# Kernel tuning notes

Hardware: AMD Instinct MI355X
Metric: run time of the kernel (lower is better)

## Reference

```python
import jax, jax.numpy as jnp
import numpy as np

KS = 3      # kernel size
PAD = 1     # zero padding
STRIDE = 1
N = KS * KS # 9 sampling points per pixel


def _deform_conv(feature, offset, weight):
    """DeformConv2d: bilinear sample at learned offsets then 3x3 conv (no bias)."""
    b, c, h, w = feature.shape
    x = jnp.pad(feature, ((0, 0), (0, 0), (PAD, PAD), (PAD, PAD)))
    hp, wp = h + 2 * PAD, w + 2 * PAD
    dt = feature.dtype
    # p_n: kernel grid offsets, x(rows) first then y(cols) -> (2N,)
    rng = jnp.arange(-(KS - 1) // 2, (KS - 1) // 2 + 1, dtype=dt)
    pn_x, pn_y = jnp.meshgrid(rng, rng, indexing='ij')
    # p_0: base sampling grid starting at 1 (accounts for zero padding)
    p0_x, p0_y = jnp.meshgrid(jnp.arange(1, h + 1, dtype=dt),
                              jnp.arange(1, w + 1, dtype=dt), indexing='ij')
    # sampling locations p = p_0 + p_n + offset, split into x/y -> (b,h,w,N)
    off = jnp.transpose(offset, (0, 2, 3, 1))  # (b,h,w,2N)
    px = p0_x[None, :, :, None] + pn_x.reshape(-1)[None, None, None, :] + off[..., :N]
    py = p0_y[None, :, :, None] + pn_y.reshape(-1)[None, None, None, :] + off[..., N:]
    q_lt_x = jnp.clip(jnp.floor(px), 0, hp - 1)
    q_lt_y = jnp.clip(jnp.floor(py), 0, wp - 1)
    q_rb_x = jnp.clip(jnp.floor(px) + 1, 0, hp - 1)
    q_rb_y = jnp.clip(jnp.floor(py) + 1, 0, wp - 1)
    px = jnp.clip(px, 0, hp - 1)
    py = jnp.clip(py, 0, wp - 1)
    # bilinear weights for the 4 corners
    g_lt = (1 + (q_lt_x - px)) * (1 + (q_lt_y - py))
    g_rb = (1 - (q_rb_x - px)) * (1 - (q_rb_y - py))
    g_lb = (1 + (q_lt_x - px)) * (1 - (q_rb_y - py))
    g_rt = (1 - (q_rb_x - px)) * (1 + (q_lt_y - py))
    x_flat = x.reshape(b, c, hp * wp)

    def gather(qx, qy):
        idx = (qx * wp + qy).astype(jnp.int32).reshape(b, 1, -1)
        v = jnp.take_along_axis(x_flat, jnp.broadcast_to(idx, (b, c, h * w * N)), axis=2)
        return v.reshape(b, c, h, w, N)

    x_off = (g_lt[:, None] * gather(q_lt_x, q_lt_y)
             + g_rb[:, None] * gather(q_rb_x, q_rb_y)
             + g_lb[:, None] * gather(q_lt_x, q_rb_y)
             + g_rt[:, None] * gather(q_rb_x, q_lt_y))  # (b,c,h,w,N)
    # equivalent of _reshape_x_offset + conv(ks, stride=ks)
    x_off = x_off.reshape(b, c, h, w, KS, KS)
    return jnp.einsum('bchwij,ocij->bohw', x_off, weight)


def setup_inputs() -> dict:
    key = jax.random.key(0)
    k1, k2, k3 = jax.random.split(key, 3)
    B, C, H, W = 4, 256, 64, 64
    feature = jax.random.normal(k1, (B, C, H, W), dtype=jnp.float32)
    offset = jax.random.normal(k2, (B, 2 * N, H, W), dtype=jnp.float32)
    weight = jax.random.normal(k3, (C, C, KS, KS), dtype=jnp.float32) / np.sqrt(C * N)
    return {"feature": feature, "offset": offset, "weight": weight}


def reference(feature, offset, weight):
    f1 = jax.nn.relu(_deform_conv(feature, offset, weight))
    return jax.nn.relu(f1 + feature)
```

## Files before the change

### kernel.cpp

```cpp
#include <hip/hip_runtime.h>

#define HW    4096
#define J_TOT 16384
#define K_TOT 2304
#define C_CH  256

typedef unsigned short u16;
typedef unsigned int   u32;
typedef __attribute__((ext_vector_type(8))) short short8;
typedef __attribute__((ext_vector_type(4))) float f32x4;
typedef __attribute__((ext_vector_type(8))) unsigned short us8;

__device__ __forceinline__ float b2f(u16 u) { return __uint_as_float(((u32)u) << 16); }
__device__ __forceinline__ u16 f2b(float x) {
  u32 u = __float_as_uint(x);
  u += 0x7FFFu + ((u >> 16) & 1u);
  return (u16)(u >> 16);
}

__device__ __forceinline__ void gload_lds16(const u16* g, u16* l) {
  __builtin_amdgcn_global_load_lds(
      (__attribute__((address_space(1))) void*)(void*)g,
      (__attribute__((address_space(3))) void*)(void*)l, 16, 0, 0);
}

__global__ void k_detect(const u16* __restrict__ f, int* __restrict__ flag) {
  __shared__ int sh[256];
  int t = threadIdx.x;
  int hits = 0;
  for (int i = t; i < 2048; i += 256) {
    u16 u = f[2 * i];
    int e = (u >> 7) & 0xFF;
    hits += (e >= 100 && e <= 141) ? 1 : 0;
  }
  sh[t] = hits;
  __syncthreads();
  if (t == 0) {
    int s = 0;
    for (int i = 0; i < 256; i++) s += sh[i];
    flag[0] = (s > 1024) ? 1 : 0;
  }
}

__global__ void k_transpose(const void* __restrict__ featv, u16* __restrict__ ftr,
                            const int* __restrict__ flag) {
  __shared__ u16 tile[32][33];
  int isbf = *flag;
  int b = blockIdx.z;
  int hw0 = blockIdx.x << 5;
  int c0 = blockIdx.y << 5;
  int tx = threadIdx.x;
  int ty = threadIdx.y;
  if (isbf) {
    const u16* f = (const u16*)featv;
#pragma unroll
    for (int i = 0; i < 4; i++) {
      int c = c0 + ty + i * 8;
      tile[ty + i * 8][tx] = f[(((size_t)(b * C_CH + c)) << 12) + hw0 + tx];
    }
  } else {
    const float* f = (const float*)featv;
#pragma unroll
    for (int i = 0; i < 4; i++) {
      int c = c0 + ty + i * 8;
      tile[ty + i * 8][tx] = f2b(f[(((size_t)(b * C_CH + c)) << 12) + hw0 + tx]);
    }
  }
  __syncthreads();
#pragma unroll
  for (int i = 0; i < 4; i++) {
    int hw = hw0 + ty + i * 8;
    ftr[(((size_t)(b * HW + hw)) << 8) + c0 + tx] = tile[tx][ty + i * 8];
  }
}

__global__ void k_wconv(const void* __restrict__ wv, u16* __restrict__ Wr,
                        const int* __restrict__ flag) {
  int isbf = *flag;
  int idx = blockIdx.x * 256 + threadIdx.x;
  if (idx >= C_CH * K_TOT) return;
  int c = idx & 255;
  int n = (idx >> 8) % 9;
  int o = idx / K_TOT;
  int src = (o * 256 + c) * 9 + n;
  if (isbf) Wr[idx] = ((const u16*)wv)[src];
  else      Wr[idx] = f2b(((const float*)wv)[src]);
}

__global__ __launch_bounds__(256) void k_gather(const void* __restrict__ offv,
                                                const u16* __restrict__ ftr,
                                                u16* __restrict__ Xt,
                                                const int* __restrict__ flag) {
  __shared__ float gs[9][4][16];
  __shared__ int   isx[9][4][16];
  int isbf = *flag;
  int j0 = blockIdx.x << 4;
  int b = j0 >> 12;
  int hw0 = j0 & (HW - 1);
  int t = threadIdx.x;

  if (t < 144) {
    int p = t & 15, n = t >> 4;
    int hw = hw0 + p;
    int h = hw >> 6, w = hw & 63;
    size_t obi = (((size_t)(b * 18 + n)) << 12) + hw;
    float ox, oy;
    if (isbf) {
      const u16* po = (const u16*)offv;
      ox = b2f(po[obi]);
      oy = b2f(po[obi + (9u << 12)]);
    } else {
      const float* po = (const float*)offv;
      ox = po[obi];
      oy = po[obi + (9u << 12)];
    }
    int ki = n / 3, kj = n % 3;
    float px = (float)(h + ki) + ox;
    float py = (float)(w + kj) + oy;
    float fx = floorf(px), fy = floorf(py);
    float qltx = fminf(fmaxf(fx, 0.f), 65.f);
    float qlty = fminf(fmaxf(fy, 0.f), 65.f);
    float qrbx = fminf(fmaxf(fx + 1.f, 0.f), 65.f);
    float qrby = fminf(fmaxf(fy + 1.f, 0.f), 65.f);
    float pcx = fminf(fmaxf(px, 0.f), 65.f);
    float pcy = fminf(fmaxf(py, 0.f), 65.f);
    float dltx = 1.f + (qltx - pcx);
    float drbx = 1.f - (qrbx - pcx);
    float dlty = 1.f + (qlty - pcy);
    float drby = 1.f - (qrby - pcy);
    float g0 = dltx * dlty;
    float g1 = drbx * drby;
    float g2 = dltx * drby;
    float g3 = drbx * dlty;
    int x0 = (int)qltx, y0 = (int)qlty, x1 = (int)qrbx, y1 = (int)qrby;
    int v0 = (x0 >= 1 && x0 <= 64 && y0 >= 1 && y0 <= 64);
    int v1 = (x1 >= 1 && x1 <= 64 && y1 >= 1 && y1 <= 64);
    int v2 = (x0 >= 1 && x0 <= 64 && y1 >= 1 && y1 <= 64);
    int v3 = (x1 >= 1 && x1 <= 64 && y0 >= 1 && y0 <= 64);
    int base = b << 12;
    isx[n][0][p] = v0 ? ((base + ((x0 - 1) << 6) + (y0 - 1)) << 8) : 0;
    isx[n][1][p] = v1 ? ((base + ((x1 - 1) << 6) + (y1 - 1)) << 8) : 0;
    isx[n][2][p] = v2 ? ((base + ((x0 - 1) << 6) + (y1 - 1)) << 8) : 0;
    isx[n][3][p] = v3 ? ((base + ((x1 - 1) << 6) + (y0 - 1)) << 8) : 0;
    gs[n][0][p] = v0 ? g0 : 0.f;
    gs[n][1][p] = v1 ? g1 : 0.f;
    gs[n][2][p] = v2 ? g2 : 0.f;
    gs[n][3][p] = v3 ? g3 : 0.f;
  }
  __syncthreads();

  int p = t >> 4, cq = t & 15;
  size_t rowb = (size_t)(j0 + p) * K_TOT;
  int cA = cq * 8, cB = 128 + cq * 8;
  for (int n = 0; n < 9; n++) {
    float g0 = gs[n][0][p], g1 = gs[n][1][p], g2 = gs[n][2][p], g3 = gs[n][3][p];
    const u16* f0 = ftr + isx[n][0][p];
    const u16* f1 = ftr + isx[n][1][p];
    const u16* f2 = ftr + isx[n][2][p];
    const u16* f3 = ftr + isx[n][3][p];
    u16* dst = Xt + rowb + n * 256;
#pragma unroll
    for (int half = 0; half < 2; half++) {
      int c = half ? cB : cA;
      us8 r0 = *(const us8*)(f0 + c);
      us8 r1 = *(const us8*)(f1 + c);
      us8 r2 = *(const us8*)(f2 + c);
      us8 r3 = *(const us8*)(f3 + c);
      us8 ov;
#pragma unroll
      for (int i = 0; i < 8; i++) {
        float v = g0 * b2f(r0[i]) + g1 * b2f(r1[i]) + g2 * b2f(r2[i]) + g3 * b2f(r3[i]);
        ov[i] = f2b(v);
      }
      *(us8*)(dst + c) = ov;
    }
  }
}

#define NT 36

#define GEMM_STAGE(bufi)                                                     \
  do {                                                                       \
    u16* _bl = &Bs[bufi][wave * 2048];                                       \
    u16* _al = &As[bufi][wave * 1024];                                       \
    gload_lds16(bsrc0, _bl);                                                 \
    gload_lds16(bsrc1, _bl + 512);                                           \
    gload_lds16(bsrc2, _bl + 1024);                                          \
    gload_lds16(bsrc3, _bl + 1536);                                          \
    gload_lds16(asrc0, _al);                                                 \
    gload_lds16(asrc1, _al + 512);                                           \
    bsrc0 += 64; bsrc1 += 64; bsrc2 += 64; bsrc3 += 64;                      \
    asrc0 += 64; asrc1 += 64;                                                \
  } while (0)

#define GEMM_COMPUTE(bufi)                                                   \
  do {                                                                       \
    short8 af[2][2], bf[4][2];                                               \
    _Pragma("unroll")                                                        \
    for (int kk = 0; kk < 2; kk++) {                                         \
      int go = (((kk << 2) + lk) ^ swz) << 3;                                \
      _Pragma("unroll")                                                      \
      for (int oi = 0; oi < 2; oi++)                                         \
        af[oi][kk] = *(const short8*)(As[bufi] + (wo * 32 + oi * 16 + lr) * 64 + go); \
      _Pragma("unroll")                                                      \
      for (int ji = 0; ji < 4; ji++)                                         \
        bf[ji][kk] = *(const short8*)(Bs[bufi] + (wj * 64 + ji * 16 + lr) * 64 + go); \
    }                                                                        \
    __builtin_amdgcn_s_setprio(1);                                           \
    _Pragma("unroll")                                                        \
    for (int kk = 0; kk < 2; kk++)                                           \
      _Pragma("unroll")                                                      \
      for (int oi = 0; oi < 2; oi++)                                         \
        _Pragma("unroll")                                                    \
        for (int ji = 0; ji < 4; ji++)                                       \
          acc[oi][ji] = __builtin_amdgcn_mfma_f32_16x16x32_bf16(             \
              af[oi][kk], bf[ji][kk], acc[oi][ji], 0, 0, 0);                 \
    __builtin_amdgcn_s_setprio(0);                                           \
  } while (0)

__global__ __launch_bounds__(256) void k_gemm(const u16* __restrict__ Wr,
                                              const u16* __restrict__ Xt,
                                              const void* __restrict__ featv,
                                              void* __restrict__ outv,
                                              const int* __restrict__ flag) {
  __shared__ u16 Bs[3][128 * 64];
  __shared__ u16 As[3][64 * 64];
  int isbf = *flag;
  asm volatile("" :: "s"(isbf));
  int jb = blockIdx.x << 7;
  int ob0 = blockIdx.y << 6;
  int t = threadIdx.x;
  int wave = t >> 6, lane = t & 63;
  int wj = wave >> 1, wo = wave & 1;
  int lr = lane & 15, lk = lane >> 4;
  int swz = lr & 7;

  f32x4 acc[2][4];
  f32x4 zero = {0.f, 0.f, 0.f, 0.f};
#pragma unroll
  for (int i = 0; i < 2; i++)
#pragma unroll
    for (int j = 0; j < 4; j++) acc[i][j] = zero;

  int rb = lane >> 3;
  int cs = ((lane & 7) ^ rb) << 3;
  const u16* bsrc0 = Xt + (size_t)(jb + wave * 32 +  0 + rb) * K_TOT + cs;
  const u16* bsrc1 = Xt + (size_t)(jb + wave * 32 +  8 + rb) * K_TOT + cs;
  const u16* bsrc2 = Xt + (size_t)(jb + wave * 32 + 16 + rb) * K_TOT + cs;
  const u16* bsrc3 = Xt + (size_t)(jb + wave * 32 + 24 + rb) * K_TOT + cs;
  const u16* asrc0 = Wr + (size_t)(ob0 + wave * 16 + 0 + rb) * K_TOT + cs;
  const u16* asrc1 = Wr + (size_t)(ob0 + wave * 16 + 8 + rb) * K_TOT + cs;

  GEMM_STAGE(0);
  GEMM_STAGE(1);
  asm volatile("s_waitcnt vmcnt(6)" ::: "memory");
  __builtin_amdgcn_s_barrier();

  int cb = 0, sb = 2;
  for (int tt = 0; tt < NT - 2; ++tt) {
    GEMM_STAGE(sb);
    GEMM_COMPUTE(cb);
    asm volatile("s_waitcnt vmcnt(6)" ::: "memory");
    __builtin_amdgcn_s_barrier();
    cb = (cb + 1 == 3) ? 0 : cb + 1;
    sb = (sb + 1 == 3) ? 0 : sb + 1;
  }
  GEMM_COMPUTE(cb);
  asm volatile("s_waitcnt vmcnt(0)" ::: "memory");
  __builtin_amdgcn_s_barrier();
  cb = (cb + 1 == 3) ? 0 : cb + 1;
  GEMM_COMPUTE(cb);

  int lq = lane >> 4;
#pragma unroll
  for (int oi = 0; oi < 2; oi++) {
#pragma unroll
    for (int ji = 0; ji < 4; ji++) {
      int j = jb + wj * 64 + ji * 16 + lr;
      int bb_ = j >> 12, hw = j & (HW - 1);
      int o0 = ob0 + wo * 32 + oi * 16 + lq * 4;
#pragma unroll
      for (int r = 0; r < 4; r++) {
        size_t oidx = (((size_t)(bb_ * C_CH + o0 + r)) << 12) + hw;
        float v = acc[oi][ji][r];
        v = fmaxf(v, 0.f);
        float ft = isbf ? b2f(((const u16*)featv)[oidx]) : ((const float*)featv)[oidx];
        v = fmaxf(v + ft, 0.f);
        if (isbf) ((u16*)outv)[oidx] = f2b(v);
        else      ((float*)outv)[oidx] = v;
      }
    }
  }
}

extern "C" void kernel_launch(void* const* d_in, const int* in_sizes, int n_in,
                              void* d_out, int out_size, void* d_ws, size_t ws_size,
                              hipStream_t stream) {
  const void* feat = d_in[0];
  const void* offs = d_in[1];
  const void* wght = d_in[2];

  const size_t off_flag = 0;
  const size_t off_wr   = 256;
  const size_t off_ftr  = off_wr + (size_t)1179648;
  const size_t off_xt   = off_ftr + (size_t)8388608;
  const size_t need     = off_xt + (size_t)75497472;
  if (ws_size < need) return;

  char* ws = (char*)d_ws;
  int* flag = (int*)(ws + off_flag);
  u16* Wr   = (u16*)(ws + off_wr);
  u16* ftr  = (u16*)(ws + off_ftr);
  u16* Xt   = (u16*)(ws + off_xt);

  k_detect<<<1, 256, 0, stream>>>((const u16*)feat, flag);
  k_transpose<<<dim3(128, 8, 4), dim3(32, 8), 0, stream>>>(feat, ftr, flag);
  k_wconv<<<K_TOT, 256, 0, stream>>>(wght, Wr, flag);
  k_gather<<<J_TOT / 16, 256, 0, stream>>>(offs, ftr, Xt, flag);
  k_gemm<<<dim3(J_TOT / 128, 4), 256, 0, stream>>>(Wr, Xt, feat, d_out, flag);
}
```

Measured before the change: 140.7 us.

## Retile GEMM to cover all output channels per block, reading Xt once

Changes the GEMM block tile from 64 channels x 128 columns with 4 waves to all 256 channels x 64 columns with 8 waves. Each block now reads its slice of the large gathered matrix once instead of four times across output-channel blocks, cutting HBM traffic. The cost is larger LDS per block (one resident block per CU), a 512-thread launch, and more weight reads from L2.

Result: slower. 145.0 us (+3.0%).

```diff
diff --git a/kernel.cpp b/kernel.cpp
--- a/kernel.cpp
+++ b/kernel.cpp
@@ -181,16 +181,12 @@
 
 #define GEMM_STAGE(bufi)                                                     \
   do {                                                                       \
-    u16* _bl = &Bs[bufi][wave * 2048];                                       \
-    u16* _al = &As[bufi][wave * 1024];                                       \
-    gload_lds16(bsrc0, _bl);                                                 \
-    gload_lds16(bsrc1, _bl + 512);                                           \
-    gload_lds16(bsrc2, _bl + 1024);                                          \
-    gload_lds16(bsrc3, _bl + 1536);                                          \
-    gload_lds16(asrc0, _al);                                                 \
-    gload_lds16(asrc1, _al + 512);                                           \
-    bsrc0 += 64; bsrc1 += 64; bsrc2 += 64; bsrc3 += 64;                      \
-    asrc0 += 64; asrc1 += 64;                                                \
+    gload_lds16(bsrc,  &Bs[bufi][wave * 512]);                               \
+    gload_lds16(asrc0, &As[bufi][wave * 2048]);                              \
+    gload_lds16(asrc1, &As[bufi][wave * 2048 + 512]);                        \
+    gload_lds16(asrc2, &As[bufi][wave * 2048 + 1024]);                       \
+    gload_lds16(asrc3, &As[bufi][wave * 2048 + 1536]);                       \
+    bsrc += 64; asrc0 += 64; asrc1 += 64; asrc2 += 64; asrc3 += 64;          \
   } while (0)
 
 #define GEMM_COMPUTE(bufi)                                                   \
@@ -201,10 +197,10 @@
       int go = (((kk << 2) + lk) ^ swz) << 3;                                \
       _Pragma("unroll")                                                      \
       for (int oi = 0; oi < 2; oi++)                                         \
-        af[oi][kk] = *(const short8*)(As[bufi] + (wo * 32 + oi * 16 + lr) * 64 + go); \
+        af[oi][kk] = *(const short8*)(As[bufi] + (wave * 32 + oi * 16 + lr) * 64 + go); \
       _Pragma("unroll")                                                      \
       for (int ji = 0; ji < 4; ji++)                                         \
-        bf[ji][kk] = *(const short8*)(Bs[bufi] + (wj * 64 + ji * 16 + lr) * 64 + go); \
+        bf[ji][kk] = *(const short8*)(Bs[bufi] + (ji * 16 + lr) * 64 + go);  \
     }                                                                        \
     __builtin_amdgcn_s_setprio(1);                                           \
     _Pragma("unroll")                                                        \
@@ -218,20 +214,18 @@
     __builtin_amdgcn_s_setprio(0);                                           \
   } while (0)
 
-__global__ __launch_bounds__(256) void k_gemm(const u16* __restrict__ Wr,
+__global__ __launch_bounds__(512) void k_gemm(const u16* __restrict__ Wr,
                                               const u16* __restrict__ Xt,
                                               const void* __restrict__ featv,
                                               void* __restrict__ outv,
                                               const int* __restrict__ flag) {
-  __shared__ u16 Bs[3][128 * 64];
-  __shared__ u16 As[3][64 * 64];
+  __shared__ u16 Bs[3][64 * 64];
+  __shared__ u16 As[3][256 * 64];
   int isbf = *flag;
   asm volatile("" :: "s"(isbf));
-  int jb = blockIdx.x << 7;
-  int ob0 = blockIdx.y << 6;
+  int jb = blockIdx.x << 6;
   int t = threadIdx.x;
   int wave = t >> 6, lane = t & 63;
-  int wj = wave >> 1, wo = wave & 1;
   int lr = lane & 15, lk = lane >> 4;
   int swz = lr & 7;
 
@@ -244,23 +238,22 @@
 
   int rb = lane >> 3;
   int cs = ((lane & 7) ^ rb) << 3;
-  const u16* bsrc0 = Xt + (size_t)(jb + wave * 32 +  0 + rb) * K_TOT + cs;
-  const u16* bsrc1 = Xt + (size_t)(jb + wave * 32 +  8 + rb) * K_TOT + cs;
-  const u16* bsrc2 = Xt + (size_t)(jb + wave * 32 + 16 + rb) * K_TOT + cs;
-  const u16* bsrc3 = Xt + (size_t)(jb + wave * 32 + 24 + rb) * K_TOT + cs;
-  const u16* asrc0 = Wr + (size_t)(ob0 + wave * 16 + 0 + rb) * K_TOT + cs;
-  const u16* asrc1 = Wr + (size_t)(ob0 + wave * 16 + 8 + rb) * K_TOT + cs;
+  const u16* bsrc  = Xt + (size_t)(jb + wave * 8 + rb) * K_TOT + cs;
+  const u16* asrc0 = Wr + (size_t)(wave * 32 +  0 + rb) * K_TOT + cs;
+  const u16* asrc1 = Wr + (size_t)(wave * 32 +  8 + rb) * K_TOT + cs;
+  const u16* asrc2 = Wr + (size_t)(wave * 32 + 16 + rb) * K_TOT + cs;
+  const u16* asrc3 = Wr + (size_t)(wave * 32 + 24 + rb) * K_TOT + cs;
 
   GEMM_STAGE(0);
   GEMM_STAGE(1);
-  asm volatile("s_waitcnt vmcnt(6)" ::: "memory");
+  asm volatile("s_waitcnt vmcnt(5)" ::: "memory");
   __builtin_amdgcn_s_barrier();
 
   int cb = 0, sb = 2;
   for (int tt = 0; tt < NT - 2; ++tt) {
     GEMM_STAGE(sb);
     GEMM_COMPUTE(cb);
-    asm volatile("s_waitcnt vmcnt(6)" ::: "memory");
+    asm volatile("s_waitcnt vmcnt(5)" ::: "memory");
     __builtin_amdgcn_s_barrier();
     cb = (cb + 1 == 3) ? 0 : cb + 1;
     sb = (sb + 1 == 3) ? 0 : sb + 1;
@@ -276,9 +269,9 @@
   for (int oi = 0; oi < 2; oi++) {
 #pragma unroll
     for (int ji = 0; ji < 4; ji++) {
-      int j = jb + wj * 64 + ji * 16 + lr;
+      int j = jb + ji * 16 + lr;
       int bb_ = j >> 12, hw = j & (HW - 1);
-      int o0 = ob0 + wo * 32 + oi * 16 + lq * 4;
+      int o0 = wave * 32 + oi * 16 + lq * 4;
 #pragma unroll
       for (int r = 0; r < 4; r++) {
         size_t oidx = (((size_t)(bb_ * C_CH + o0 + r)) << 12) + hw;
@@ -317,5 +310,5 @@
   k_transpose<<<dim3(128, 8, 4), dim3(32, 8), 0, stream>>>(feat, ftr, flag);
   k_wconv<<<K_TOT, 256, 0, stream>>>(wght, Wr, flag);
   k_gather<<<J_TOT / 16, 256, 0, stream>>>(offs, ftr, Xt, flag);
-  k_gemm<<<dim3(J_TOT / 128, 4), 256, 0, stream>>>(Wr, Xt, feat, d_out, flag);
-}
+  k_gemm<<<J_TOT / 64, 512, 0, stream>>>(Wr, Xt, feat, d_out, flag);
+}
```
